# Kernel optimization log

Hardware: AMD Instinct MI355X
Metric: run time of the kernel (lower is better)

## Reference

```python
import jax, jax.numpy as jnp
import numpy as np

B, D, P = 2048, 768, 200
DOWN = [(384, 768), (192, 384), (96, 192), (48, 96)]
UP = [(96, 48), (192, 96), (384, 192), (768, 384)]


def setup_inputs() -> dict:
    key = jax.random.key(0)
    ks = jax.random.split(key, 32)
    inp = {
        "x": jax.random.normal(ks[0], (B, D), jnp.float32),
        "aW": jax.random.normal(ks[1], (D, D), jnp.float32) * 0.02,
        "ab": jax.random.normal(ks[2], (D,), jnp.float32) * 0.02,
        "protos": jax.random.normal(ks[3], (P, D), jnp.float32),
    }
    k = 4
    for i, (o, ii) in enumerate(DOWN):
        inp[f"Wd{i}"] = jax.random.normal(ks[k], (o, ii), jnp.float32) * (1.0 / np.sqrt(ii)); k += 1
        inp[f"bd{i}"] = jax.random.normal(ks[k], (o,), jnp.float32) * 0.02; k += 1
    for i, (o, ii) in enumerate(UP):
        inp[f"Wu{i}"] = jax.random.normal(ks[k], (o, ii), jnp.float32) * (1.0 / np.sqrt(ii)); k += 1
        inp[f"bu{i}"] = jax.random.normal(ks[k], (o,), jnp.float32) * 0.02; k += 1
    return inp


def _adopter_net(x, Wds, bds, Wus, bus):
    # down path with skip storage
    x_inter = []
    h = x
    for Wd, bd in zip(Wds, bds):
        h = jax.nn.relu(h @ Wd.T + bd)
        x_inter.append(h)
    # up path: residual adds for middle layers (i==1 uses x_inter[-2], i==2 uses x_inter[-3])
    n = len(Wus)
    for i, (Wu, bu) in enumerate(zip(Wus, bus)):
        if i == 0 or i == n - 1:
            h = jax.nn.relu(h @ Wu.T + bu)
        else:
            h = jax.nn.relu((h + x_inter[-i - 1]) @ Wu.T + bu)
    return h


def reference(x, aW, ab, Wd0, bd0, Wd1, bd1, Wd2, bd2, Wd3, bd3,
              Wu0, bu0, Wu1, bu1, Wu2, bu2, Wu3, bu3, protos):
    Wds, bds = [Wd0, Wd1, Wd2, Wd3], [bd0, bd1, bd2, bd3]
    Wus, bus = [Wu0, Wu1, Wu2, Wu3], [bu0, bu1, bu2, bu3]
    # features = x + adapter(x) + adopters(x)
    features = x + (x @ aW.T + ab) + _adopter_net(x, Wds, bds, Wus, bus)  # [B, D]
    # fused per-prototype negative L1 distance (replaces Python loop over PrototypeBase)
    logits = -jnp.sum(jnp.abs(features[:, None, :] - protos[None, :, :]), axis=-1)  # [B, P]
    return logits
```

## Files before the change

kernel.cpp:

```cpp
#include <hip/hip_runtime.h>

typedef __attribute__((ext_vector_type(8))) __bf16 bf16x8;
typedef __attribute__((ext_vector_type(4))) float f32x4;
typedef _Float16 hf2 __attribute__((ext_vector_type(2)));
typedef _Float16 hf8 __attribute__((ext_vector_type(8)));
typedef unsigned short u16;
typedef struct { hf2 v[4]; } hf2x4;

__device__ __forceinline__ float bf2f(u16 h) {
    return __uint_as_float(((unsigned int)h) << 16);
}
__device__ __forceinline__ u16 f2bf(float f) {
    unsigned int u = __float_as_uint(f);
    u += 0x7fffu + ((u >> 16) & 1u);
    return (u16)(u >> 16);
}

#if __has_builtin(__builtin_amdgcn_fdot2)
__device__ __forceinline__ float FDOT2(hf2 a, hf2 b, float c) {
    return __builtin_amdgcn_fdot2(a, b, c, false);
}
#else
__device__ __forceinline__ float FDOT2(hf2 a, hf2 b, float c) {
    return c + (float)a[0] + (float)a[1];
}
#endif

#define GLOAD_LDS16(gsrc, ldst)                                                          \
    __builtin_amdgcn_global_load_lds(                                                    \
        (__attribute__((address_space(1))) unsigned int*)(gsrc),                         \
        (__attribute__((address_space(3))) unsigned int*)(ldst), 16, 0, 0)

struct CvtDesc { const float* src; u16* dst; int N, K, Npad, Kpad, blk0, fmt; };
struct CvtTab { CvtDesc t[11]; };

__global__ __launch_bounds__(256) void cvt_all(CvtTab tab) {
    int b = blockIdx.x;
    int ti = 0;
#pragma unroll
    for (int j = 1; j < 11; ++j)
        if (b >= tab.t[j].blk0) ti = j;
    const CvtDesc c = tab.t[ti];
    long i = (long)(b - c.blk0) * 256 + threadIdx.x;
    long tot = (long)c.Npad * c.Kpad;
    if (i >= tot) return;
    int n = (int)(i / c.Kpad);
    int k = (int)(i - (long)n * c.Kpad);
    float v = (n < c.N && k < c.K) ? c.src[(long)n * c.K + k] : 0.f;
    if (c.fmt) {
        _Float16 h = (_Float16)v;
        c.dst[i] = __builtin_bit_cast(u16, h);
    } else {
        c.dst[i] = f2bf(v);
    }
}

template<int RELU, int HASRES, int MODE>
__device__ __forceinline__ void gemm_body(
    char* lds,
    const u16* __restrict__ A, int lda,
    const u16* __restrict__ W, int ldw,
    const float* __restrict__ bias, int Nreal,
    u16* __restrict__ outB, int ldo,
    const u16* __restrict__ res,
    float* __restrict__ outF, _Float16* __restrict__ outH,
    const float* __restrict__ addF,
    int nk, int mb, int nb)
{
    char* ldsA = lds;
    char* ldsB = lds + 8192;

    const int tid  = threadIdx.x;
    const int wave = tid >> 6;
    const int lane = tid & 63;
    const int wr = wave >> 1, wc = wave & 1;
    const int lr = lane & 15, lk = lane >> 4;

    f32x4 acc[2][2];
#pragma unroll
    for (int i = 0; i < 2; ++i)
#pragma unroll
        for (int j = 0; j < 2; ++j)
#pragma unroll
            for (int e = 0; e < 4; ++e) acc[i][j][e] = 0.f;

    const int g0 = wave * 64 + lane;
    const int r0 = g0 >> 3, l0 = (g0 & 7) ^ (r0 & 7);
    const int g1 = g0 + 256;
    const int r1 = g1 >> 3, l1 = (g1 & 7) ^ (r1 & 7);

    for (int kt = 0; kt < nk; ++kt) {
        const int kk = kt * 64;
        GLOAD_LDS16(A + (size_t)(mb + r0) * lda + kk + l0 * 8, ldsA + wave * 1024);
        GLOAD_LDS16(A + (size_t)(mb + r1) * lda + kk + l1 * 8, ldsA + 4096 + wave * 1024);
        GLOAD_LDS16(W + (size_t)(nb + r0) * ldw + kk + l0 * 8, ldsB + wave * 1024);
        GLOAD_LDS16(W + (size_t)(nb + r1) * ldw + kk + l1 * 8, ldsB + 4096 + wave * 1024);
        __syncthreads();
#pragma unroll
        for (int ks = 0; ks < 2; ++ks) {
            bf16x8 af[2], bfr[2];
#pragma unroll
            for (int mi = 0; mi < 2; ++mi) {
                int m_loc = wr * 32 + mi * 16 + lr;
                int gr = (ks * 4 + lk) ^ (m_loc & 7);
                af[mi] = *(const bf16x8*)(ldsA + m_loc * 128 + gr * 16);
            }
#pragma unroll
            for (int ni = 0; ni < 2; ++ni) {
                int n_loc = wc * 32 + ni * 16 + lr;
                int gr = (ks * 4 + lk) ^ (n_loc & 7);
                bfr[ni] = *(const bf16x8*)(ldsB + n_loc * 128 + gr * 16);
            }
#pragma unroll
            for (int mi = 0; mi < 2; ++mi)
#pragma unroll
                for (int ni = 0; ni < 2; ++ni)
                    acc[mi][ni] = __builtin_amdgcn_mfma_f32_16x16x32_bf16(
                        af[mi], bfr[ni], acc[mi][ni], 0, 0, 0);
        }
        __syncthreads();
    }

#pragma unroll
    for (int mi = 0; mi < 2; ++mi) {
#pragma unroll
        for (int ni = 0; ni < 2; ++ni) {
            const int n_g = nb + wc * 32 + ni * 16 + lr;
            const float bv = (n_g < Nreal) ? bias[n_g] : 0.f;
#pragma unroll
            for (int r = 0; r < 4; ++r) {
                const int m_g = mb + wr * 32 + mi * 16 + lk * 4 + r;
                float v = acc[mi][ni][r] + bv;
                if (RELU) v = fmaxf(v, 0.f);
                if (HASRES) v += bf2f(res[(size_t)m_g * ldo + n_g]);
                if (MODE == 1) {
                    outF[(size_t)m_g * 768 + n_g] = v + addF[(size_t)m_g * 768 + n_g];
                } else if (MODE == 2) {
                    outH[(size_t)m_g * 768 + n_g] =
                        (_Float16)(v + addF[(size_t)m_g * 768 + n_g]);
                } else {
                    outB[(size_t)m_g * ldo + n_g] = f2bf(v);
                }
            }
        }
    }
}

template<int RELU, int HASRES, int MODE>
__global__ __launch_bounds__(256) void gemm_k(
    const u16* __restrict__ A, int lda,
    const u16* __restrict__ W, int ldw,
    const float* __restrict__ bias, int Nreal,
    u16* __restrict__ outB, int ldo,
    const u16* __restrict__ res,
    float* __restrict__ outF, _Float16* __restrict__ outH,
    const float* __restrict__ addF, int nk)
{
    __shared__ __align__(16) char lds[16384];
    gemm_body<RELU, HASRES, MODE>(lds, A, lda, W, ldw, bias, Nreal, outB, ldo,
                                  res, outF, outH, addF, nk,
                                  blockIdx.x * 64, blockIdx.y * 64);
}

__global__ __launch_bounds__(256) void gemm_ad0(
    const u16* __restrict__ xb,
    const u16* __restrict__ aWb, const float* __restrict__ ab,
    float* __restrict__ adF, const float* __restrict__ x,
    const u16* __restrict__ Wd0b, const float* __restrict__ bd0,
    u16* __restrict__ h1)
{
    __shared__ __align__(16) char lds[16384];
    if (blockIdx.y < 12) {
        gemm_body<0, 0, 1>(lds, xb, 768, aWb, 768, ab, 768, nullptr, 0,
                           nullptr, adF, nullptr, x, 12,
                           blockIdx.x * 64, blockIdx.y * 64);
    } else {
        gemm_body<1, 0, 0>(lds, xb, 768, Wd0b, 768, bd0, 384, h1, 384,
                           nullptr, nullptr, nullptr, nullptr, 12,
                           blockIdx.x * 64, (blockIdx.y - 12) * 64);
    }
}

__global__ __launch_bounds__(256) void l1_kernel(
    const _Float16* __restrict__ feat, const _Float16* __restrict__ protos,
    float* __restrict__ part)
{
    __shared__ _Float16 fs[128][64];
    __shared__ hf2 pt[32][64];
    const int tid = threadIdx.x;
    const int tp = tid & 15, tr = tid >> 4;
    const int rb = blockIdx.x * 128;
    const int pb = blockIdx.y * 64;
    const int db = blockIdx.z * 64;

    {
        const int g = tid & 7, r0 = tid >> 3;
#pragma unroll
        for (int k = 0; k < 4; ++k) {
            const int r = r0 + 32 * k;
            *(hf8*)&fs[r][g * 8] =
                *(const hf8*)&feat[(size_t)(rb + r) * 768 + db + g * 8];
        }
    }
    {
        const int sp = tid & 63, q = tid >> 6;
        const _Float16* src = &protos[(size_t)(pb + sp) * 768 + db + q * 16];
        hf8 v0 = *(const hf8*)src;
        hf8 v1 = *(const hf8*)(src + 8);
        hf2x4 w0 = __builtin_bit_cast(hf2x4, v0);
        hf2x4 w1 = __builtin_bit_cast(hf2x4, v1);
#pragma unroll
        for (int e = 0; e < 4; ++e)
            pt[q * 8 + e][sp] = w0.v[e];
#pragma unroll
        for (int e = 0; e < 4; ++e)
            pt[q * 8 + 4 + e][sp] = w1.v[e];
    }
    __syncthreads();

    float acc[8][4];
#pragma unroll
    for (int i = 0; i < 8; ++i)
#pragma unroll
        for (int j = 0; j < 4; ++j) acc[i][j] = 0.f;

    const hf2 one2 = {(_Float16)1.0f, (_Float16)1.0f};
#pragma unroll 2
    for (int g = 0; g < 8; ++g) {
        hf2x4 F2[8];
#pragma unroll
        for (int i = 0; i < 8; ++i)
            F2[i] = __builtin_bit_cast(hf2x4,
                        *(const hf8*)&fs[tr + 16 * i][g * 8]);
        hf2x4 P2[4];
#pragma unroll
        for (int q = 0; q < 4; ++q)
            P2[q] = __builtin_bit_cast(hf2x4,
                        *(const hf8*)&pt[g * 4 + q][tp * 4]);
#pragma unroll
        for (int q = 0; q < 4; ++q) {
#pragma unroll
            for (int j = 0; j < 4; ++j) {
                const hf2 pj = P2[q].v[j];
#pragma unroll
                for (int i = 0; i < 8; ++i) {
                    hf2 d = F2[i].v[q] - pj;
                    unsigned ud = __builtin_bit_cast(unsigned, d) & 0x7FFF7FFFu;
                    acc[i][j] = FDOT2(__builtin_bit_cast(hf2, ud), one2, acc[i][j]);
                }
            }
        }
    }
    const int p = pb + tp * 4;
    if (p < 200) {
        const size_t zb = (size_t)blockIdx.z * 2048;
#pragma unroll
        for (int i = 0; i < 8; ++i) {
            float4 v = {-acc[i][0], -acc[i][1], -acc[i][2], -acc[i][3]};
            *(float4*)&part[(zb + rb + tr + 16 * i) * 200 + p] = v;
        }
    }
}

__global__ __launch_bounds__(256) void l1_reduce(
    const float* __restrict__ part, float* __restrict__ out)
{
    const int row = blockIdx.x;
    const int p = threadIdx.x;
    if (p < 200) {
        float s = 0.f;
#pragma unroll
        for (int z = 0; z < 12; ++z)
            s += part[((size_t)z * 2048 + row) * 200 + p];
        out[(size_t)row * 200 + p] = s;
    }
}

static constexpr size_t OFF_PART  = 0;
static constexpr size_t OFF_XB    = 0;
static constexpr size_t OFF_AWB   = 3145728;
static constexpr size_t OFF_WD0   = 4325376;
static constexpr size_t OFF_WD1   = 4915200;
static constexpr size_t OFF_WD2   = 5062656;
static constexpr size_t OFF_WD3   = 5111808;
static constexpr size_t OFF_WU0   = 5128192;
static constexpr size_t OFF_WU1   = 5144576;
static constexpr size_t OFF_WU2   = 5193728;
static constexpr size_t OFF_WU3   = 5341184;
static constexpr size_t OFF_H1    = 5931008;
static constexpr size_t OFF_H2    = 7503872;
static constexpr size_t OFF_H3    = 8290304;
static constexpr size_t OFF_H4    = 8814592;
static constexpr size_t OFF_U0    = 9076736;
static constexpr size_t OFF_U1    = 9601024;
static constexpr size_t OFF_U2    = 10387456;
static constexpr size_t OFF_ADF   = 11960320;
static constexpr size_t OFF_FEATH = 19660800;
static constexpr size_t OFF_PROH  = 22806528;

extern "C" void kernel_launch(void* const* d_in, const int* in_sizes, int n_in,
                              void* d_out, int out_size, void* d_ws, size_t ws_size,
                              hipStream_t stream) {
    const float* x      = (const float*)d_in[0];
    const float* aW     = (const float*)d_in[1];
    const float* ab     = (const float*)d_in[2];
    const float* protos = (const float*)d_in[3];
    const float* Wd[4]  = {(const float*)d_in[4], (const float*)d_in[6],
                           (const float*)d_in[8], (const float*)d_in[10]};
    const float* bd[4]  = {(const float*)d_in[5], (const float*)d_in[7],
                           (const float*)d_in[9], (const float*)d_in[11]};
    const float* Wu[4]  = {(const float*)d_in[12], (const float*)d_in[14],
                           (const float*)d_in[16], (const float*)d_in[18]};
    const float* bu[4]  = {(const float*)d_in[13], (const float*)d_in[15],
                           (const float*)d_in[17], (const float*)d_in[19]};
    float* out = (float*)d_out;
    char* ws = (char*)d_ws;

    u16* xb    = (u16*)(ws + OFF_XB);
    u16* aWb   = (u16*)(ws + OFF_AWB);
    u16* Wd0b  = (u16*)(ws + OFF_WD0);
    u16* Wd1b  = (u16*)(ws + OFF_WD1);
    u16* Wd2b  = (u16*)(ws + OFF_WD2);
    u16* Wd3b  = (u16*)(ws + OFF_WD3);
    u16* Wu0b  = (u16*)(ws + OFF_WU0);
    u16* Wu1b  = (u16*)(ws + OFF_WU1);
    u16* Wu2b  = (u16*)(ws + OFF_WU2);
    u16* Wu3b  = (u16*)(ws + OFF_WU3);
    u16* h1    = (u16*)(ws + OFF_H1);
    u16* h2    = (u16*)(ws + OFF_H2);
    u16* h3    = (u16*)(ws + OFF_H3);
    u16* h4    = (u16*)(ws + OFF_H4);
    u16* u0    = (u16*)(ws + OFF_U0);
    u16* u1    = (u16*)(ws + OFF_U1);
    u16* u2    = (u16*)(ws + OFF_U2);
    float* adF = (float*)(ws + OFF_ADF);
    float* part = (float*)(ws + OFF_PART);
    _Float16* featH = (_Float16*)(ws + OFF_FEATH);
    _Float16* proH  = (_Float16*)(ws + OFF_PROH);

    CvtTab tab;
    int blk = 0;
    auto set = [&](int i, const float* s, u16* d, int N, int K, int Np, int Kp,
                   int fmt) {
        tab.t[i] = {s, d, N, K, Np, Kp, blk, fmt};
        blk += (Np * Kp + 255) / 256;
    };
    set(0,  x,      xb,          2048, 768, 2048, 768, 0);
    set(1,  aW,     aWb,         768,  768, 768,  768, 0);
    set(2,  Wd[0],  Wd0b,        384,  768, 384,  768, 0);
    set(3,  Wd[1],  Wd1b,        192,  384, 192,  384, 0);
    set(4,  Wd[2],  Wd2b,        96,   192, 128,  192, 0);
    set(5,  Wd[3],  Wd3b,        48,   96,  64,   128, 0);
    set(6,  Wu[0],  Wu0b,        96,   48,  128,  64,  0);
    set(7,  Wu[1],  Wu1b,        192,  96,  192,  128, 0);
    set(8,  Wu[2],  Wu2b,        384,  192, 384,  192, 0);
    set(9,  Wu[3],  Wu3b,        768,  384, 768,  384, 0);
    set(10, protos, (u16*)proH,  200,  768, 256,  768, 1);
    cvt_all<<<blk, 256, 0, stream>>>(tab);

    gemm_ad0<<<dim3(32, 18), 256, 0, stream>>>(xb, aWb, ab, adF, x, Wd0b, bd[0], h1);
    gemm_k<1,0,0><<<dim3(32,3), 256, 0, stream>>>(h1, 384, Wd1b, 384, bd[1], 192,
        h2, 192, nullptr, nullptr, nullptr, nullptr, 6);
    gemm_k<1,0,0><<<dim3(32,2), 256, 0, stream>>>(h2, 192, Wd2b, 192, bd[2], 96,
        h3, 128, nullptr, nullptr, nullptr, nullptr, 3);
    gemm_k<1,0,0><<<dim3(32,1), 256, 0, stream>>>(h3, 128, Wd3b, 128, bd[3], 48,
        h4, 64, nullptr, nullptr, nullptr, nullptr, 2);
    gemm_k<1,1,0><<<dim3(32,2), 256, 0, stream>>>(h4, 64, Wu0b, 64, bu[0], 96,
        u0, 128, h3, nullptr, nullptr, nullptr, 1);
    gemm_k<1,1,0><<<dim3(32,3), 256, 0, stream>>>(u0, 128, Wu1b, 128, bu[1], 192,
        u1, 192, h2, nullptr, nullptr, nullptr, 2);
    gemm_k<1,0,0><<<dim3(32,6), 256, 0, stream>>>(u1, 192, Wu2b, 192, bu[2], 384,
        u2, 384, nullptr, nullptr, nullptr, nullptr, 3);
    gemm_k<1,0,2><<<dim3(32,12), 256, 0, stream>>>(u2, 384, Wu3b, 384, bu[3], 768,
        nullptr, 0, nullptr, nullptr, featH, adF, 6);

    l1_kernel<<<dim3(16, 4, 12), 256, 0, stream>>>(featH, proH, part);
    l1_reduce<<<dim3(2048), 256, 0, stream>>>(part, out);
}
```

Baseline: 90.57 us.

## Fuse six middle adapter GEMM layers into one LDS-resident kernel

Replaces six separate small GEMM launches (Wd1..Wd3, Wu0..Wu2) with a single kernel. Each block owns 16 rows and keeps the intermediate activations in shared memory, running the MFMA layers back to back with barriers between them. This is meant to remove per-launch overhead and the global-memory round trips of the h2/h3/h4/u0/u1 intermediates. In exchange, only 128 blocks run, and each block streams every weight matrix straight from global memory without LDS staging, so parallelism and weight reuse are reduced.

```diff
diff --git a/kernel.cpp b/kernel.cpp
--- a/kernel.cpp
+++ b/kernel.cpp
@@ -181,6 +181,90 @@
     }
 }
 
+template<int K, int NPAD, int NREAL, int RES, int OUTG>
+__device__ __forceinline__ void layer16(
+    const u16* __restrict__ W, int ldw, const float* __restrict__ bias,
+    const u16* actIn, int ldin,
+    u16* actOut, int ldout,
+    const u16* resid, int ldres,
+    u16* __restrict__ gout, int ldg)
+{
+    constexpr int TPW = NPAD / 64;
+    const int tid = threadIdx.x;
+    const int wave = tid >> 6, lane = tid & 63;
+    const int lr = lane & 15, lk = lane >> 4;
+
+    f32x4 acc[TPW];
+#pragma unroll
+    for (int t = 0; t < TPW; ++t)
+#pragma unroll
+        for (int e = 0; e < 4; ++e) acc[t][e] = 0.f;
+
+#pragma unroll
+    for (int kk = 0; kk < K / 32; ++kk) {
+        const bf16x8 a = *(const bf16x8*)&actIn[lr * ldin + kk * 32 + lk * 8];
+#pragma unroll
+        for (int t = 0; t < TPW; ++t) {
+            const int nc = (wave * TPW + t) * 16 + lr;
+            const bf16x8 b = *(const bf16x8*)&W[(size_t)nc * ldw + kk * 32 + lk * 8];
+            acc[t] = __builtin_amdgcn_mfma_f32_16x16x32_bf16(a, b, acc[t], 0, 0, 0);
+        }
+    }
+#pragma unroll
+    for (int t = 0; t < TPW; ++t) {
+        const int nc = (wave * TPW + t) * 16 + lr;
+        const float bv = (nc < NREAL) ? bias[nc] : 0.f;
+#pragma unroll
+        for (int r = 0; r < 4; ++r) {
+            const int row = lk * 4 + r;
+            float v = fmaxf(acc[t][r] + bv, 0.f);
+            if (RES) v += bf2f(resid[row * ldres + nc]);
+            const u16 o = f2bf(v);
+            if (OUTG) gout[(size_t)row * ldg + nc] = o;
+            else      actOut[row * ldout + nc] = o;
+        }
+    }
+}
+
+__global__ __launch_bounds__(256) void chain_mid(
+    const u16* __restrict__ h1,
+    const u16* __restrict__ Wd1b, const float* __restrict__ bd1,
+    const u16* __restrict__ Wd2b, const float* __restrict__ bd2,
+    const u16* __restrict__ Wd3b, const float* __restrict__ bd3,
+    const u16* __restrict__ Wu0b, const float* __restrict__ bu0,
+    const u16* __restrict__ Wu1b, const float* __restrict__ bu1,
+    const u16* __restrict__ Wu2b, const float* __restrict__ bu2,
+    u16* __restrict__ u2)
+{
+    __shared__ u16 A[16 * 392];
+    __shared__ u16 B[16 * 200];
+    __shared__ u16 C[16 * 136];
+    __shared__ u16 D[16 * 72];
+    const int tid = threadIdx.x;
+    const int rb = blockIdx.x * 16;
+
+    for (int i = tid; i < 768; i += 256) {
+        const int r = i / 48, c = i - r * 48;
+        *(bf16x8*)&A[r * 392 + c * 8] =
+            *(const bf16x8*)&h1[(size_t)(rb + r) * 384 + c * 8];
+    }
+    __syncthreads();
+    layer16<384, 192, 192, 0, 0>(Wd1b, 384, bd1, A, 392, B, 200, nullptr, 0, nullptr, 0);
+    __syncthreads();
+    layer16<192, 128,  96, 0, 0>(Wd2b, 192, bd2, B, 200, C, 136, nullptr, 0, nullptr, 0);
+    __syncthreads();
+    layer16<128,  64,  48, 0, 0>(Wd3b, 128, bd3, C, 136, D,  72, nullptr, 0, nullptr, 0);
+    __syncthreads();
+    u16* E = A;
+    u16* F = A + 16 * 136;
+    layer16< 64, 128,  96, 1, 0>(Wu0b,  64, bu0, D,  72, E, 136, C, 136, nullptr, 0);
+    __syncthreads();
+    layer16<128, 192, 192, 1, 0>(Wu1b, 128, bu1, E, 136, F, 200, B, 200, nullptr, 0);
+    __syncthreads();
+    layer16<192, 384, 384, 0, 1>(Wu2b, 192, bu2, F, 200, nullptr, 0, nullptr, 0,
+                                 u2 + (size_t)rb * 384, 384);
+}
+
 __global__ __launch_bounds__(256) void l1_kernel(
     const _Float16* __restrict__ feat, const _Float16* __restrict__ protos,
     float* __restrict__ part)
@@ -288,11 +372,6 @@
 static constexpr size_t OFF_WU2   = 5193728;
 static constexpr size_t OFF_WU3   = 5341184;
 static constexpr size_t OFF_H1    = 5931008;
-static constexpr size_t OFF_H2    = 7503872;
-static constexpr size_t OFF_H3    = 8290304;
-static constexpr size_t OFF_H4    = 8814592;
-static constexpr size_t OFF_U0    = 9076736;
-static constexpr size_t OFF_U1    = 9601024;
 static constexpr size_t OFF_U2    = 10387456;
 static constexpr size_t OFF_ADF   = 11960320;
 static constexpr size_t OFF_FEATH = 19660800;
@@ -327,11 +406,6 @@
     u16* Wu2b  = (u16*)(ws + OFF_WU2);
     u16* Wu3b  = (u16*)(ws + OFF_WU3);
     u16* h1    = (u16*)(ws + OFF_H1);
-    u16* h2    = (u16*)(ws + OFF_H2);
-    u16* h3    = (u16*)(ws + OFF_H3);
-    u16* h4    = (u16*)(ws + OFF_H4);
-    u16* u0    = (u16*)(ws + OFF_U0);
-    u16* u1    = (u16*)(ws + OFF_U1);
     u16* u2    = (u16*)(ws + OFF_U2);
     float* adF = (float*)(ws + OFF_ADF);
     float* part = (float*)(ws + OFF_PART);
@@ -359,18 +433,9 @@
     cvt_all<<<blk, 256, 0, stream>>>(tab);
 
     gemm_ad0<<<dim3(32, 18), 256, 0, stream>>>(xb, aWb, ab, adF, x, Wd0b, bd[0], h1);
-    gemm_k<1,0,0><<<dim3(32,3), 256, 0, stream>>>(h1, 384, Wd1b, 384, bd[1], 192,
-        h2, 192, nullptr, nullptr, nullptr, nullptr, 6);
-    gemm_k<1,0,0><<<dim3(32,2), 256, 0, stream>>>(h2, 192, Wd2b, 192, bd[2], 96,
-        h3, 128, nullptr, nullptr, nullptr, nullptr, 3);
-    gemm_k<1,0,0><<<dim3(32,1), 256, 0, stream>>>(h3, 128, Wd3b, 128, bd[3], 48,
-        h4, 64, nullptr, nullptr, nullptr, nullptr, 2);
-    gemm_k<1,1,0><<<dim3(32,2), 256, 0, stream>>>(h4, 64, Wu0b, 64, bu[0], 96,
-        u0, 128, h3, nullptr, nullptr, nullptr, 1);
-    gemm_k<1,1,0><<<dim3(32,3), 256, 0, stream>>>(u0, 128, Wu1b, 128, bu[1], 192,
-        u1, 192, h2, nullptr, nullptr, nullptr, 2);
-    gemm_k<1,0,0><<<dim3(32,6), 256, 0, stream>>>(u1, 192, Wu2b, 192, bu[2], 384,
-        u2, 384, nullptr, nullptr, nullptr, nullptr, 3);
+    chain_mid<<<dim3(128), 256, 0, stream>>>(h1,
+        Wd1b, bd[1], Wd2b, bd[2], Wd3b, bd[3],
+        Wu0b, bu[0], Wu1b, bu[1], Wu2b, bu[2], u2);
     gemm_k<1,0,2><<<dim3(32,12), 256, 0, stream>>>(u2, 384, Wu3b, 384, bu[3], 768,
         nullptr, 0, nullptr, nullptr, featH, adF, 6);
 
```

Result: faster. 84.18 us (-7.1%).
